# Kernel optimization log

Measured on AMD Instinct MI355X. Metric: run time of the kernel, lower is better.

The kernel has to match this reference:

```python
import jax, jax.numpy as jnp
import numpy as np

B, N, C, H = 8, 1025, 1024, 16
DH = C // H
HID = 4 * C
EPS = 1e-5
NEG = -65504.0


def _ln(x, g, b):
    mu = jnp.mean(x, axis=-1, keepdims=True)
    var = jnp.mean(jnp.square(x - mu), axis=-1, keepdims=True)
    return (x - mu) * jax.lax.rsqrt(var + EPS) * g + b


def setup_inputs() -> dict:
    key = jax.random.key(0)
    ks = jax.random.split(key, 12)
    s = 0.02
    return {
        "x": jax.random.normal(ks[0], (B, N, C), jnp.float32),
        "rel_pos_bias": jax.random.normal(ks[1], (H, N, N), jnp.float32),
        "attn_mask": jnp.zeros((B, N, N), jnp.bool_),
        "ln1_g": jnp.ones((C,), jnp.float32),
        "ln1_b": jnp.zeros((C,), jnp.float32),
        "qkv_w": jax.random.normal(ks[2], (C, 3 * C), jnp.float32) * s,
        "qkv_b": jnp.zeros((3 * C,), jnp.float32),
        "proj_w": jax.random.normal(ks[3], (C, C), jnp.float32) * s,
        "proj_b": jnp.zeros((C,), jnp.float32),
        "ln2_g": jnp.ones((C,), jnp.float32),
        "ln2_b": jnp.zeros((C,), jnp.float32),
        "fc1_w": jax.random.normal(ks[4], (C, HID), jnp.float32) * s,
        "fc1_b": jnp.zeros((HID,), jnp.float32),
        "fc2_w": jax.random.normal(ks[5], (HID, C), jnp.float32) * s,
        "fc2_b": jnp.zeros((C,), jnp.float32),
    }


def reference(x, rel_pos_bias, attn_mask, ln1_g, ln1_b, qkv_w, qkv_b,
              proj_w, proj_b, ln2_g, ln2_b, fc1_w, fc1_b, fc2_w, fc2_b):
    scale = DH ** -0.5
    # --- attention branch ---
    h = _ln(x, ln1_g, ln1_b)
    qkv = (h @ qkv_w + qkv_b).reshape(B, N, 3, H, DH)
    q, k, v = [jnp.transpose(qkv[:, :, i], (0, 2, 1, 3)) for i in range(3)]  # [B,H,N,DH]
    attn = jnp.einsum('bhnd,bhmd->bhnm', q * scale, k)
    attn = jnp.where(attn_mask[:, None], NEG, attn)
    attn = attn + rel_pos_bias  # [H,N,N] broadcasts over batch
    attn_wo_softmax = attn
    a = jax.nn.softmax(attn, axis=-1)
    o = jnp.einsum('bhnm,bhmd->bhnd', a, v)
    o = jnp.transpose(o, (0, 2, 1, 3)).reshape(B, N, C)
    o = o @ proj_w + proj_b
    x = x + o
    # --- MLP branch ---
    h2 = _ln(x, ln2_g, ln2_b)
    h2 = jax.nn.gelu(h2 @ fc1_w + fc1_b, approximate=False)
    x = x + (h2 @ fc2_w + fc2_b)
    return (x, attn_wo_softmax)
```

## Files before the change

### kernel.cpp

```cpp
#include <hip/hip_runtime.h>
#include <math.h>

typedef unsigned short u16;
typedef unsigned char u8;
typedef unsigned int u32;
typedef __attribute__((ext_vector_type(4))) float f32x4;
typedef __attribute__((ext_vector_type(4), aligned(4))) float f32x4u;
typedef __attribute__((ext_vector_type(8))) short s16x8;

#define DEV __device__ __forceinline__

constexpr int BB = 8, NN = 1025, CC = 1024, HH = 16;
constexpr int NP  = 1152;
constexpr int MP  = 8320;
constexpr int TOK = BB * NN;
constexpr int MW  = 36;
constexpr float NEGV = -65504.f;

DEV u16 f2bf(float f){ union { float f; unsigned u; } v; v.f = f; return (u16)((v.u + 0x7fffu + ((v.u >> 16) & 1u)) >> 16); }
DEV float bf2f(u16 u){ union { float f; unsigned u; } v; v.u = (unsigned)u << 16; return v.f; }
DEV u32 cvt_pk_bf16(float lo_, float hi_){
  u32 r; asm("v_cvt_pk_bf16_f32 %0, %1, %2" : "=v"(r) : "v"(lo_), "v"(hi_)); return r;
}

struct __align__(8) us4 { u16 x, y, z, w; };

typedef const __attribute__((address_space(1))) void gv_t;
typedef __attribute__((address_space(3))) void lv_t;
DEV void gload16(const void* g, void* l){
  __builtin_amdgcn_global_load_lds((gv_t*)g, (lv_t*)l, 16, 0, 0);
}

__launch_bounds__(256)
__global__ void cvt_transpose(const float* __restrict__ W, u16* __restrict__ Wt, int K, int Nn){
  __shared__ float tile[32][33];
  const int n0 = blockIdx.x * 32, k0 = blockIdx.y * 32;
  const int tx = threadIdx.x & 31, ty = threadIdx.x >> 5;
#pragma unroll
  for (int i = 0; i < 4; i++)
    tile[ty + i * 8][tx] = W[(size_t)(k0 + ty + i * 8) * Nn + n0 + tx];
  __syncthreads();
#pragma unroll
  for (int i = 0; i < 4; i++){
    const int n = n0 + ty + i * 8;
    Wt[(size_t)n * K + k0 + tx] = f2bf(tile[tx][ty + i * 8]);
  }
}

__launch_bounds__(256)
__global__ void ln_kernel(const float* __restrict__ x, const float* __restrict__ g,
                          const float* __restrict__ b, u16* __restrict__ out, int validRows){
  const int row = blockIdx.x, tid = threadIdx.x;
  const size_t base = (size_t)row * CC + tid * 4;
  if (row >= validRows){ us4 z{0,0,0,0}; *(us4*)(out + base) = z; return; }
  f32x4u v = *(const f32x4u*)(x + base);
  float s  = v[0] + v[1] + v[2] + v[3];
  float ss = v[0]*v[0] + v[1]*v[1] + v[2]*v[2] + v[3]*v[3];
#pragma unroll
  for (int o = 32; o; o >>= 1){ s += __shfl_xor(s, o, 64); ss += __shfl_xor(ss, o, 64); }
  __shared__ float ps[4], pq[4];
  if ((tid & 63) == 0){ ps[tid >> 6] = s; pq[tid >> 6] = ss; }
  __syncthreads();
  s  = ps[0] + ps[1] + ps[2] + ps[3];
  ss = pq[0] + pq[1] + pq[2] + pq[3];
  const float mu = s * (1.f / CC);
  const float rs = rsqrtf(ss * (1.f / CC) - mu * mu + 1e-5f);
  f32x4u gv = *(const f32x4u*)(g + tid * 4);
  f32x4u bv = *(const f32x4u*)(b + tid * 4);
  us4 o;
  o.x = f2bf((v[0]-mu)*rs*gv[0] + bv[0]);
  o.y = f2bf((v[1]-mu)*rs*gv[1] + bv[1]);
  o.z = f2bf((v[2]-mu)*rs*gv[2] + bv[2]);
  o.w = f2bf((v[3]-mu)*rs*gv[3] + bv[3]);
  *(us4*)(out + base) = o;
}

template<int MODE>
__launch_bounds__(256)
__global__ void gemm_nt(const u16* __restrict__ A, const u16* __restrict__ Bt,
                        const float* __restrict__ bias, int K, int Nw,
                        const float* __restrict__ resid, float* __restrict__ fout,
                        u16* __restrict__ bout){
  __shared__ u16 As[128 * 32];
  __shared__ u16 Bs[128 * 32];
  const int tid = threadIdx.x;
  const int w = tid >> 6, l = tid & 63;
  const int wr = w >> 1, wc = w & 1;
  const int row0 = blockIdx.y * 128, col0 = blockIdx.x * 128;
  f32x4 acc[4][4] = {};
  for (int k0 = 0; k0 < K; k0 += 32){
    __syncthreads();
#pragma unroll
    for (int j = 0; j < 2; j++){
      const int ch = tid + j * 256;
      const int r = ch >> 2, co = (ch & 3) * 8;
      gload16(A  + (size_t)(row0 + r) * K + k0 + co, As + (size_t)ch * 8);
      gload16(Bt + (size_t)(col0 + r) * K + k0 + co, Bs + (size_t)ch * 8);
    }
    __syncthreads();
    s16x8 af[4], bf[4];
#pragma unroll
    for (int m = 0; m < 4; m++)
      af[m] = *(const s16x8*)(As + (wr * 64 + m * 16 + (l & 15)) * 32 + (l >> 4) * 8);
#pragma unroll
    for (int n = 0; n < 4; n++)
      bf[n] = *(const s16x8*)(Bs + (wc * 64 + n * 16 + (l & 15)) * 32 + (l >> 4) * 8);
#pragma unroll
    for (int m = 0; m < 4; m++)
#pragma unroll
      for (int n = 0; n < 4; n++)
        acc[m][n] = __builtin_amdgcn_mfma_f32_16x16x32_bf16(af[m], bf[n], acc[m][n], 0, 0, 0);
  }
#pragma unroll
  for (int m = 0; m < 4; m++){
#pragma unroll
    for (int n = 0; n < 4; n++){
      const int c = col0 + wc * 64 + n * 16 + (l & 15);
      const float bs = bias[c];
#pragma unroll
      for (int j = 0; j < 4; j++){
        const int r = row0 + wr * 64 + m * 16 + ((l >> 4) << 2) + j;
        float v = acc[m][n][j] + bs;
        if (MODE == 0){
          bout[(size_t)r * Nw + c] = f2bf(v);
        } else if (MODE == 1){
          const float xi = (r < TOK) ? resid[(size_t)r * CC + c] : 0.f;
          fout[(size_t)r * CC + c] = xi + v;
        } else if (MODE == 2){
          const float gx = 0.5f * v * (1.f + erff(v * 0.70710678118654752f));
          bout[(size_t)r * Nw + c] = f2bf(gx);
        } else {
          if (r < TOK) fout[(size_t)r * CC + c] = resid[(size_t)r * CC + c] + v;
        }
      }
    }
  }
}

__launch_bounds__(256)
__global__ void reorder_qkv(const u16* __restrict__ qkv, u16* __restrict__ q,
                            u16* __restrict__ k, u16* __restrict__ vT){
  __shared__ u16 vt[64][65];
  const int bh = blockIdx.y, b = bh >> 4, h = bh & 15;
  const int n0 = blockIdx.x * 64;
  const int tid = threadIdx.x;
  const int d = tid & 63, nl = tid >> 6;
#pragma unroll
  for (int i = 0; i < 16; i++){
    const int nlocal = nl * 16 + i;
    const int n = n0 + nlocal;
    u16 qv = 0, kv = 0, vv = 0;
    if (n < NN){
      const size_t t = (size_t)b * NN + n;
      const u16* p = qkv + t * 3072 + h * 64 + d;
      qv = f2bf(bf2f(p[0]) * 0.125f);
      kv = p[1024];
      vv = p[2048];
    }
    q[(size_t)bh * NP * 64 + (size_t)n * 64 + d] = qv;
    k[(size_t)bh * NP * 64 + (size_t)n * 64 + d] = kv;
    vt[nlocal][d] = vv;
  }
  __syncthreads();
#pragma unroll
  for (int i = 0; i < 16; i++){
    const int dd = (tid >> 6) * 16 + i;
    const int nn2 = tid & 63;
    vT[(size_t)bh * 64 * NP + (size_t)dd * NP + n0 + nn2] = vt[nn2][dd];
  }
}

__launch_bounds__(256)
__global__ void mask_pack(const u8* __restrict__ mask, u32* __restrict__ mbits){
  const int idx = blockIdx.x * 256 + threadIdx.x;
  if (idx >= BB * NP * MW) return;
  const int word = idx % MW;
  const int row  = (idx / MW) % NP;
  const int b    = idx / (MW * NP);
  u32 bits = 0;
  if (row < NN){
    const u8* mrow = mask + (size_t)b * NN * NN + (size_t)row * NN;
    const int c0 = word * 32;
    const int lim = (NN - c0 < 32) ? (NN - c0) : 32;
    for (int j = 0; j < lim; j++) bits |= (u32)(mrow[c0 + j] != 0) << j;
  }
  mbits[idx] = bits;
}

__launch_bounds__(512)
__global__ void attn_flash(const u16* __restrict__ q, const u16* __restrict__ k,
                           const u16* __restrict__ vT, const float* __restrict__ bias,
                           const u32* __restrict__ mbits,
                           float* __restrict__ S, u16* __restrict__ obuf){
  __shared__ u16 Ks[128 * 64];
  __shared__ u16 Vs[64 * 128];

  const int f = blockIdx.x;
  const int xcd = f & 7, ii = f >> 3;
  const int hl = ii / 72, rem = ii % 72;
  const int rt = rem >> 3, b = rem & 7;
  const int h = xcd * 2 + hl;
  const int bh = b * 16 + h;
  const int tid = threadIdx.x, w = tid >> 6, l = tid & 63;
  const int lg = l >> 4, lo = l & 15;
  const int row0 = rt * 128 + w * 16;
  const u16* qb = q + (size_t)bh * NP * 64;
  const u16* kb = k + (size_t)bh * NP * 64;
  const u16* vb = vT + (size_t)bh * 64 * NP;
  const float* bias_h = bias + (size_t)h * NN * NN;
  const u32* mrow_b = mbits + (size_t)b * NP * MW;
  float* Sb = S + (size_t)bh * NN * NN;

  s16x8 qf[2];
#pragma unroll
  for (int kk = 0; kk < 2; kk++)
    qf[kk] = *(const s16x8*)(qb + (size_t)(row0 + lo) * 64 + kk * 32 + lg * 8);

  float m_run = -1e30f, l_run = 0.f;
  f32x4 acc_o[4] = {};

  for (int ct = 0; ct < 9; ct++){
    const int cb = ct * 128;
    __syncthreads();
#pragma unroll
    for (int i = 0; i < 2; i++){
      const int chunk = tid + i * 512;
      const int row = chunk >> 3, cs = chunk & 7;
      const int cg = cs ^ (row & 7);
      gload16(kb + (size_t)(cb + row) * 64 + cg * 8, Ks + (size_t)chunk * 8);
    }
#pragma unroll
    for (int i = 0; i < 2; i++){
      const int chunk = tid + i * 512;
      const int row = chunk >> 4, cs = chunk & 15;
      const int cg = cs ^ (row & 15);
      gload16(vb + (size_t)row * NP + cb + cg * 8, Vs + (size_t)chunk * 8);
    }
    __syncthreads();

    f32x4 sa[8] = {};
#pragma unroll
    for (int m2 = 0; m2 < 8; m2++){
      const int rl = (m2 >> 1) * 32 + (lo >> 2) * 8 + (m2 & 1) * 4 + (lo & 3);
      const s16x8 kf0 = *(const s16x8*)(Ks + rl * 64 + ((lg ^ (rl & 7)) << 3));
      const s16x8 kf1 = *(const s16x8*)(Ks + rl * 64 + (((4 + lg) ^ (rl & 7)) << 3));
      sa[m2] = __builtin_amdgcn_mfma_f32_16x16x32_bf16(kf0, qf[0], sa[m2], 0, 0, 0);
      sa[m2] = __builtin_amdgcn_mfma_f32_16x16x32_bf16(kf1, qf[1], sa[m2], 0, 0, 0);
    }
    {
      const int qr = row0 + lo;
      if (qr < NN){
        const u32* mrp = mrow_b + (size_t)qr * MW + ct * 4;
        u32 mb[4];
#pragma unroll
        for (int i = 0; i < 4; i++) mb[i] = mrp[i];
        const float* brow = bias_h + (size_t)qr * NN;
        float* srow = Sb + (size_t)qr * NN;
#pragma unroll
        for (int m2 = 0; m2 < 8; m2++){
          const int kc0 = cb + (m2 >> 1) * 32 + lg * 8 + (m2 & 1) * 4;
          const u32 bits = mb[m2 >> 1] >> (lg * 8 + (m2 & 1) * 4);
          f32x4 a = sa[m2];
          if (kc0 + 3 < NN){
            f32x4u bv = *(const f32x4u*)(brow + kc0);
#pragma unroll
            for (int jj = 0; jj < 4; jj++){
              float v = ((bits >> jj) & 1u) ? NEGV : a[jj];
              a[jj] = v + bv[jj];
            }
            *(f32x4u*)(srow + kc0) = a;
          } else {
#pragma unroll
            for (int jj = 0; jj < 4; jj++){
              if (kc0 + jj < NN){
                float v = ((bits >> jj) & 1u) ? NEGV : a[jj];
                v += brow[kc0 + jj];
                srow[kc0 + jj] = v;
                a[jj] = v;
              } else a[jj] = -1e30f;
            }
          }
          sa[m2] = a;
        }
      } else {
        const f32x4 z = {0.f, 0.f, 0.f, 0.f};
#pragma unroll
        for (int m2 = 0; m2 < 8; m2++) sa[m2] = z;
      }
    }
    float sc;
    {
      float mt = -1e30f;
#pragma unroll
      for (int m2 = 0; m2 < 8; m2++){
        f32x4 a = sa[m2];
        mt = fmaxf(mt, fmaxf(fmaxf(a[0], a[1]), fmaxf(a[2], a[3])));
      }
      mt = fmaxf(mt, __shfl_xor(mt, 16, 64));
      mt = fmaxf(mt, __shfl_xor(mt, 32, 64));
      const float mn = fmaxf(m_run, mt);
      sc = __expf(m_run - mn);
      float p = 0.f;
#pragma unroll
      for (int m2 = 0; m2 < 8; m2++){
        f32x4 a = sa[m2];
        const float e0 = __expf(a[0] - mn), e1 = __expf(a[1] - mn);
        const float e2 = __expf(a[2] - mn), e3 = __expf(a[3] - mn);
        p += (e0 + e1) + (e2 + e3);
        sa[m2][0] = __uint_as_float(cvt_pk_bf16(e0, e1));
        sa[m2][1] = __uint_as_float(cvt_pk_bf16(e2, e3));
      }
      p += __shfl_xor(p, 16, 64);
      p += __shfl_xor(p, 32, 64);
      l_run = l_run * sc + p;
      m_run = mn;
    }
#pragma unroll
    for (int jj = 0; jj < 4; jj++){
      const float s = __shfl(sc, (l & 48) + lg * 4 + jj, 64);
#pragma unroll
      for (int nd = 0; nd < 4; nd++) acc_o[nd][jj] *= s;
    }
#pragma unroll
    for (int kc = 0; kc < 4; kc++){
      union { u32 d[4]; s16x8 v8; } af;
      af.d[0] = __float_as_uint(sa[2 * kc][0]);
      af.d[1] = __float_as_uint(sa[2 * kc][1]);
      af.d[2] = __float_as_uint(sa[2 * kc + 1][0]);
      af.d[3] = __float_as_uint(sa[2 * kc + 1][1]);
#pragma unroll
      for (int nd = 0; nd < 4; nd++){
        const int vrow = nd * 16 + lo;
        const s16x8 vf = *(const s16x8*)(Vs + vrow * 128 + (((kc * 4 + lg) ^ (vrow & 15)) << 3));
        acc_o[nd] = __builtin_amdgcn_mfma_f32_16x16x32_bf16(af.v8, vf, acc_o[nd], 0, 0, 0);
      }
    }
  }
  {
    const float li = 1.f / l_run;
#pragma unroll
    for (int jj = 0; jj < 4; jj++){
      const float il = __shfl(li, (l & 48) + lg * 4 + jj, 64);
      const int qr = row0 + lg * 4 + jj;
      if (qr < NN){
        const size_t base = ((size_t)b * NN + qr) * CC + (size_t)h * 64;
#pragma unroll
        for (int nd = 0; nd < 4; nd++)
          obuf[base + nd * 16 + lo] = f2bf(acc_o[nd][jj] * il);
      }
    }
  }
}

__launch_bounds__(256)
__global__ void zero_pad_rows(u16* __restrict__ buf){
  const size_t i = (size_t)blockIdx.x * 256 + threadIdx.x;
  buf[(size_t)TOK * CC + i] = 0;
}

extern "C" void kernel_launch(void* const* d_in, const int* in_sizes, int n_in,
                              void* d_out, int out_size, void* d_ws, size_t ws_size,
                              hipStream_t stream){
  const float* x     = (const float*)d_in[0];
  const float* rpb   = (const float*)d_in[1];
  const u8*    mask  = (const u8*)d_in[2];
  const float* ln1g  = (const float*)d_in[3];
  const float* ln1b  = (const float*)d_in[4];
  const float* qkvw  = (const float*)d_in[5];
  const float* qkvb  = (const float*)d_in[6];
  const float* projw = (const float*)d_in[7];
  const float* projb = (const float*)d_in[8];
  const float* ln2g  = (const float*)d_in[9];
  const float* ln2b  = (const float*)d_in[10];
  const float* fc1w  = (const float*)d_in[11];
  const float* fc1b  = (const float*)d_in[12];
  const float* fc2w  = (const float*)d_in[13];
  const float* fc2b  = (const float*)d_in[14];

  float* out_x = (float*)d_out;
  float* out_S = out_x + (size_t)BB * NN * CC;

  char* wsb = (char*)d_ws;
  size_t off = 0;
  auto alloc = [&](size_t bytes) -> char* {
    char* p = wsb + off; off += (bytes + 255) & ~(size_t)255; return p;
  };
  u16* h1     = (u16*)alloc((size_t)MP * CC * 2);
  u16* qkvbuf = (u16*)alloc((size_t)MP * 3072 * 2);
  u16* h3     = h1;
  u16* qkvwt  = (u16*)alloc((size_t)3072 * 1024 * 2);
  u16* projwt = (u16*)alloc((size_t)1024 * 1024 * 2);
  u16* fc1wt  = (u16*)alloc((size_t)4096 * 1024 * 2);
  u16* fc2wt  = (u16*)alloc((size_t)1024 * 4096 * 2);
  u16* qq     = (u16*)alloc((size_t)128 * NP * 64 * 2);
  u16* kk     = (u16*)alloc((size_t)128 * NP * 64 * 2);
  u16* vT     = (u16*)alloc((size_t)128 * 64 * NP * 2);
  u32* mbits  = (u32*)alloc((size_t)BB * NP * MW * 4);
  u16* obuf   = (u16*)alloc((size_t)MP * CC * 2);
  float* x1   = (float*)alloc((size_t)MP * CC * 4);
  u16* h2in   = (u16*)alloc((size_t)MP * CC * 2);

  cvt_transpose<<<dim3(3072/32, 1024/32), 256, 0, stream>>>(qkvw, qkvwt, 1024, 3072);
  cvt_transpose<<<dim3(1024/32, 1024/32), 256, 0, stream>>>(projw, projwt, 1024, 1024);
  cvt_transpose<<<dim3(4096/32, 1024/32), 256, 0, stream>>>(fc1w, fc1wt, 1024, 4096);
  cvt_transpose<<<dim3(1024/32, 4096/32), 256, 0, stream>>>(fc2w, fc2wt, 4096, 1024);
  ln_kernel<<<MP, 256, 0, stream>>>(x, ln1g, ln1b, h1, TOK);
  gemm_nt<0><<<dim3(3072/128, MP/128), 256, 0, stream>>>(h1, qkvwt, qkvb, 1024, 3072, nullptr, nullptr, qkvbuf);
  reorder_qkv<<<dim3(NP/64, 128), 256, 0, stream>>>(qkvbuf, qq, kk, vT);
  mask_pack<<<(BB * NP * MW + 255) / 256, 256, 0, stream>>>(mask, mbits);
  zero_pad_rows<<<(MP - TOK) * CC / 256, 256, 0, stream>>>(obuf);
  attn_flash<<<dim3(1152), 512, 0, stream>>>(qq, kk, vT, rpb, mbits, out_S, obuf);
  gemm_nt<1><<<dim3(1024/128, MP/128), 256, 0, stream>>>(obuf, projwt, projb, 1024, 1024, x, x1, nullptr);
  ln_kernel<<<MP, 256, 0, stream>>>(x1, ln2g, ln2b, h2in, TOK);
  gemm_nt<2><<<dim3(4096/128, MP/128), 256, 0, stream>>>(h2in, fc1wt, fc1b, 1024, 4096, nullptr, nullptr, h3);
  gemm_nt<3><<<dim3(1024/128, MP/128), 256, 0, stream>>>(h3, fc2wt, fc2b, 4096, 1024, x1, out_x, nullptr);
}
```

Baseline: 819.0 us.

## Double-buffer K/V tiles in flash attention with async prefetch

Splits the K and V shared-memory tiles into two buffers and prefetches the next column tile while the current one is consumed. Manual vmcnt waits and raw barriers replace the two __syncthreads per iteration. It also raises wave priority around the MFMA blocks. LDS use doubles to 64KB per block, which may reduce occupancy. The vmcnt(4) count assumes the other global loads in the loop (bias, mask, S stores) do not interleave with the prefetch, which is fragile.

```diff
diff --git a/kernel.cpp b/kernel.cpp
--- a/kernel.cpp
+++ b/kernel.cpp
@@ -192,8 +192,8 @@
                            const u16* __restrict__ vT, const float* __restrict__ bias,
                            const u32* __restrict__ mbits,
                            float* __restrict__ S, u16* __restrict__ obuf){
-  __shared__ u16 Ks[128 * 64];
-  __shared__ u16 Vs[64 * 128];
+  __shared__ u16 Ks[2][128 * 64];
+  __shared__ u16 Vs[2][64 * 128];
 
   const int f = blockIdx.x;
   const int xcd = f & 7, ii = f >> 3;
@@ -219,34 +219,51 @@
   float m_run = -1e30f, l_run = 0.f;
   f32x4 acc_o[4] = {};
 
-  for (int ct = 0; ct < 9; ct++){
+  auto stage = [&](int buf, int ct){
     const int cb = ct * 128;
-    __syncthreads();
 #pragma unroll
     for (int i = 0; i < 2; i++){
       const int chunk = tid + i * 512;
       const int row = chunk >> 3, cs = chunk & 7;
       const int cg = cs ^ (row & 7);
-      gload16(kb + (size_t)(cb + row) * 64 + cg * 8, Ks + (size_t)chunk * 8);
+      gload16(kb + (size_t)(cb + row) * 64 + cg * 8, Ks[buf] + (size_t)chunk * 8);
     }
 #pragma unroll
     for (int i = 0; i < 2; i++){
       const int chunk = tid + i * 512;
       const int row = chunk >> 4, cs = chunk & 15;
       const int cg = cs ^ (row & 15);
-      gload16(vb + (size_t)row * NP + cb + cg * 8, Vs + (size_t)chunk * 8);
-    }
-    __syncthreads();
+      gload16(vb + (size_t)row * NP + cb + cg * 8, Vs[buf] + (size_t)chunk * 8);
+    }
+  };
+
+  stage(0, 0);
+
+  for (int ct = 0; ct < 9; ct++){
+    const int cb = ct * 128;
+    const int cur = ct & 1;
+    if (ct < 8){
+      stage(cur ^ 1, ct + 1);
+      asm volatile("s_waitcnt vmcnt(4)" ::: "memory");
+    } else {
+      asm volatile("s_waitcnt vmcnt(0)" ::: "memory");
+    }
+    __builtin_amdgcn_s_barrier();
+    __builtin_amdgcn_sched_barrier(0);
+    const u16* KsC = Ks[cur];
+    const u16* VsC = Vs[cur];
 
     f32x4 sa[8] = {};
+    __builtin_amdgcn_s_setprio(1);
 #pragma unroll
     for (int m2 = 0; m2 < 8; m2++){
       const int rl = (m2 >> 1) * 32 + (lo >> 2) * 8 + (m2 & 1) * 4 + (lo & 3);
-      const s16x8 kf0 = *(const s16x8*)(Ks + rl * 64 + ((lg ^ (rl & 7)) << 3));
-      const s16x8 kf1 = *(const s16x8*)(Ks + rl * 64 + (((4 + lg) ^ (rl & 7)) << 3));
+      const s16x8 kf0 = *(const s16x8*)(KsC + rl * 64 + ((lg ^ (rl & 7)) << 3));
+      const s16x8 kf1 = *(const s16x8*)(KsC + rl * 64 + (((4 + lg) ^ (rl & 7)) << 3));
       sa[m2] = __builtin_amdgcn_mfma_f32_16x16x32_bf16(kf0, qf[0], sa[m2], 0, 0, 0);
       sa[m2] = __builtin_amdgcn_mfma_f32_16x16x32_bf16(kf1, qf[1], sa[m2], 0, 0, 0);
     }
+    __builtin_amdgcn_s_setprio(0);
     {
       const int qr = row0 + lo;
       if (qr < NN){
@@ -321,6 +338,7 @@
 #pragma unroll
       for (int nd = 0; nd < 4; nd++) acc_o[nd][jj] *= s;
     }
+    __builtin_amdgcn_s_setprio(1);
 #pragma unroll
     for (int kc = 0; kc < 4; kc++){
       union { u32 d[4]; s16x8 v8; } af;
@@ -331,10 +349,13 @@
 #pragma unroll
       for (int nd = 0; nd < 4; nd++){
         const int vrow = nd * 16 + lo;
-        const s16x8 vf = *(const s16x8*)(Vs + vrow * 128 + (((kc * 4 + lg) ^ (vrow & 15)) << 3));
+        const s16x8 vf = *(const s16x8*)(VsC + vrow * 128 + (((kc * 4 + lg) ^ (vrow & 15)) << 3));
         acc_o[nd] = __builtin_amdgcn_mfma_f32_16x16x32_bf16(af.v8, vf, acc_o[nd], 0, 0, 0);
       }
     }
+    __builtin_amdgcn_s_setprio(0);
+    __builtin_amdgcn_s_barrier();
+    __builtin_amdgcn_sched_barrier(0);
   }
   {
     const float li = 1.f / l_run;
```

After: 789.1 us. -3.7%, faster.
